# Kernel tuning notes

Hardware: AMD Instinct MI355X
Metric: run time of the kernel (lower is better)

The kernel has to match this reference:

```python
import jax, jax.numpy as jnp
import numpy as np
from jax import lax

B, CIN, H, W = 8, 256, 128, 128
CC, COUT = 16, 64
KH, KW = 5, 5
PT, PB = KH // 2, (KH + 1) // 2 - 1  # top/bottom pad (SAME-style)
PL, PR = KW // 2, (KW + 1) // 2 - 1


def setup_inputs() -> dict:
    key = jax.random.key(0)
    k1, k2, k3, k4 = jax.random.split(key, 4)
    x = jax.random.normal(k1, (B, CIN, H, W), dtype=jnp.float32)
    W_ext = jax.random.normal(k2, (CC, CIN, 3, 3), dtype=jnp.float32) * 0.05
    b_ext = jax.random.normal(k3, (CC,), dtype=jnp.float32) * 0.05
    W_reg = jax.random.normal(k4, (COUT, CC, KH, KW), dtype=jnp.float32) * 0.05
    return {"x": x, "W_ext": W_ext, "b_ext": b_ext, "W_reg": W_reg}


def reference(x, W_ext, b_ext, W_reg):
    # extract_input: Conv2d(in->corr_channels, 3x3, pad=1)
    f = lax.conv_general_dilated(
        x, W_ext, window_strides=(1, 1), padding=[(1, 1), (1, 1)],
        dimension_numbers=("NCHW", "OIHW", "NCHW"))
    f = f + b_ext[None, :, None, None]  # (B, CC, H, W)

    # Local autocorrelation: corr[b,c,h,w,di,dj] = f[b,c,h,w] * f_pad[b,c,h+di,w+dj]
    fp = jnp.pad(f, ((0, 0), (0, 0), (PT, PB), (PL, PR)))
    # stack shifted views over the fixed kh*kw offsets (small constant loop)
    patches = jnp.stack(
        [fp[:, :, i:i + H, j:j + W] for i in range(KH) for j in range(KW)],
        axis=-1)  # (B, CC, H, W, KH*KW)
    corr = f[..., None] * patches  # (B, CC, H, W, KH*KW) cost volume

    vec = jnp.einsum("bchwk,ock->bohw", corr, W_reg.reshape(COUT, CC, KH * KW))
    return vec  # (B, COUT, H, W)
```

## Files before the change

kernel.cpp:

```cpp
#include <hip/hip_runtime.h>

#define B_    8
#define CIN_  256
#define H_    128
#define W_    128
#define CC_   16
#define COUT_ 64
#define HFP_  132
#define HW_   (H_ * W_)

#define XS_STRIDE 1634
#define XS_BUF    (4 * XS_STRIDE)

typedef _Float16 half8 __attribute__((ext_vector_type(8)));
typedef float float4v __attribute__((ext_vector_type(4)));

__global__ void repack_w1(const float* __restrict__ Wext, _Float16* __restrict__ Wa1) {
    int i = blockIdx.x * 256 + threadIdx.x;
    if (i >= 9 * 8 * 64 * 8) return;
    int j    = i & 7;
    int lane = (i >> 3) & 63;
    int blk  = (i >> 9) & 7;
    int tap  = i >> 12;
    int cc   = lane & 15;
    int cin  = blk * 32 + (lane >> 4) * 8 + j;
    Wa1[i] = (_Float16)Wext[cc * (CIN_ * 9) + cin * 9 + tap];
}

__global__ void repack_w2(const float* __restrict__ Wreg, _Float16* __restrict__ Wa2) {
    int u = blockIdx.x * 256 + threadIdx.x;
    if (u >= 4 * 13 * 64 * 8) return;
    int j    = u & 7;
    int lane = (u >> 3) & 63;
    int su   = u >> 9;
    int s    = su % 13;
    int g    = su / 13;
    int q    = lane >> 4;
    int kk   = 2 * s + (q >> 1);
    int c    = (q & 1) * 8 + j;
    int o    = g * 16 + (lane & 15);
    float v  = (kk < 25) ? Wreg[o * (CC_ * 25) + c * 25 + kk] : 0.0f;
    Wa2[u] = (_Float16)v;
}

__global__ __launch_bounds__(256, 4) void conv_fused(
    const float* __restrict__ x, const _Float16* __restrict__ Wa1,
    const float* __restrict__ bext, _Float16* __restrict__ fpad)
{
    __shared__ _Float16 xs[2 * XS_BUF];
    __shared__ _Float16 lt[4][32][16];

    const int lane = threadIdx.x;
    const int wv   = threadIdx.y;
    const int tid  = wv * 64 + lane;
    const int n    = lane & 15;
    const int q    = lane >> 4;

    const int f  = blockIdx.x + 4 * blockIdx.y + 128 * blockIdx.z;
    const int b  = f & 7;
    const int wt = (f >> 3) & 3;
    const int ht = f >> 5;
    const int h0 = ht * 4;
    const int w0 = wt * 32;

    int  goff[4];
    int  loff[4];
    bool vld[4];
    bool act[4];
#pragma unroll
    for (int p = 0; p < 4; ++p) {
        int u = p * 256 + tid;
        act[p] = (u < 816);
        if (!act[p]) u = 0;
        const int col  = u % 34;
        const int pair = u / 34;
        const int row  = pair % 6;
        const int c8   = pair / 6;
        const int hh = h0 - 1 + row;
        const int ww = w0 - 1 + col;
        vld[p] = (hh >= 0) && (hh < H_) && (ww >= 0) && (ww < W_);
        const int hc = hh < 0 ? 0 : (hh > H_ - 1 ? H_ - 1 : hh);
        const int wc = ww < 0 ? 0 : (ww > W_ - 1 ? W_ - 1 : ww);
        goff[p] = (c8 * 8) * HW_ + hc * W_ + wc;
        loff[p] = c8 * XS_STRIDE + (row * 34 + col) * 8;
    }

    const float* xb = x + (size_t)b * (CIN_ * HW_);
    float4v acc[2] = {};

#pragma unroll
    for (int p = 0; p < 4; ++p) {
        if (act[p]) {
            half8 hv;
#pragma unroll
            for (int j = 0; j < 8; ++j) {
                const float v = xb[goff[p] + j * HW_];
                hv[j] = (_Float16)(vld[p] ? v : 0.0f);
            }
            *(half8*)(xs + loff[p]) = hv;
        }
    }

    float pf[4][8];
    for (int chunk = 0; chunk < 8; ++chunk) {
        __syncthreads();
        const int cur = chunk & 1;

        if (chunk < 7) {
            const float* xc = xb + (size_t)(chunk + 1) * (32 * HW_);
#pragma unroll
            for (int p = 0; p < 4; ++p) {
                if (act[p]) {
#pragma unroll
                    for (int j = 0; j < 8; ++j)
                        pf[p][j] = xc[goff[p] + j * HW_];
                }
            }
            __builtin_amdgcn_sched_barrier(0);
        }

        const _Float16* wchunk = Wa1 + (size_t)chunk * 512 + lane * 8;
        const _Float16* xsb    = xs + cur * XS_BUF + q * XS_STRIDE + (wv * 34 + n) * 8;
#pragma unroll
        for (int r = 0; r < 3; ++r) {
#pragma unroll
            for (int s = 0; s < 3; ++s) {
                const half8 af = *(const half8*)(wchunk + (r * 3 + s) * 4096);
#pragma unroll
                for (int st = 0; st < 2; ++st) {
                    const half8 bf = *(const half8*)(xsb + (r * 34 + s + st * 16) * 8);
                    acc[st] = __builtin_amdgcn_mfma_f32_16x16x32_f16(af, bf, acc[st], 0, 0, 0);
                }
            }
        }

        if (chunk < 7) {
            _Float16* xd = xs + (cur ^ 1) * XS_BUF;
#pragma unroll
            for (int p = 0; p < 4; ++p) {
                if (act[p]) {
                    half8 hv;
#pragma unroll
                    for (int j = 0; j < 8; ++j)
                        hv[j] = (_Float16)(vld[p] ? pf[p][j] : 0.0f);
                    *(half8*)(xd + loff[p]) = hv;
                }
            }
        }
    }

    float bias[4];
#pragma unroll
    for (int rr = 0; rr < 4; ++rr) bias[rr] = bext[q * 4 + rr];

#pragma unroll
    for (int st = 0; st < 2; ++st) {
#pragma unroll
        for (int rr = 0; rr < 4; ++rr) {
            lt[wv][st * 16 + n][q * 4 + rr] = (_Float16)(acc[st][rr] + bias[rr]);
        }
    }
    __syncthreads();

    const half8 o = *(const half8*)&lt[wv][lane >> 1][(lane & 1) * 8];
    _Float16* dst = fpad + (((size_t)b * HFP_ + (h0 + wv + 2)) * HFP_ + (w0 + (lane >> 1) + 2)) * 16
                    + (lane & 1) * 8;
    *(half8*)dst = o;
}

__global__ __launch_bounds__(256, 4) void corr_mfma(
    const _Float16* __restrict__ fpad, const _Float16* __restrict__ Wa2,
    float* __restrict__ out)
{
    const int lane = threadIdx.x;
    const int wv   = threadIdx.y;
    const int n    = lane & 15;
    const int q    = lane >> 4;

    const int f  = blockIdx.x + 2 * blockIdx.y + 256 * blockIdx.z;
    const int b  = f & 7;
    const int xt = (f >> 3) & 1;
    const int h  = f >> 4;
    const int w0 = xt * 64 + wv * 16;

    const _Float16* fb = fpad + ((size_t)b * HFP_ + h) * (HFP_ * 16);
    const int coff = (q & 1) * 8;

    const half8 ctr = *(const half8*)(fb + (size_t)(2 * HFP_ + (w0 + n + 2)) * 16 + coff);
    half8 sh[13];
#pragma unroll
    for (int s = 0; s < 13; ++s) {
        int kk = 2 * s + (q >> 1);
        if (kk > 24) kk = 24;
        const int ki = kk / 5, kj = kk % 5;
        sh[s] = *(const half8*)(fb + (size_t)(ki * HFP_ + (w0 + n + kj)) * 16 + coff);
    }
    __builtin_amdgcn_sched_barrier(0);

    half8 corr[13];
#pragma unroll
    for (int s = 0; s < 13; ++s) corr[s] = ctr * sh[s];

    float4v acc[4] = {};
    const _Float16* wp = Wa2 + (size_t)lane * 8;
#pragma unroll
    for (int s = 0; s < 13; ++s) {
#pragma unroll
        for (int g = 0; g < 4; ++g) {
            const half8 wf = *(const half8*)(wp + (size_t)(g * 13 + s) * 512);
            acc[g] = __builtin_amdgcn_mfma_f32_16x16x32_f16(wf, corr[s], acc[g], 0, 0, 0);
        }
    }

#pragma unroll
    for (int g = 0; g < 4; ++g) {
#pragma unroll
        for (int rr = 0; rr < 4; ++rr) {
            const int o = g * 16 + q * 4 + rr;
            out[((size_t)(b * COUT_ + o) * H_ + h) * W_ + (w0 + n)] = acc[g][rr];
        }
    }
}

extern "C" void kernel_launch(void* const* d_in, const int* in_sizes, int n_in,
                              void* d_out, int out_size, void* d_ws, size_t ws_size,
                              hipStream_t stream) {
    const float* x    = (const float*)d_in[0];
    const float* Wext = (const float*)d_in[1];
    const float* bext = (const float*)d_in[2];
    const float* Wreg = (const float*)d_in[3];
    float* out = (float*)d_out;

    char* ws = (char*)d_ws;
    _Float16* fpad = (_Float16*)ws;
    _Float16* Wa1  = (_Float16*)(ws + 4460544);
    _Float16* Wa2  = (_Float16*)(ws + 4460544 + 73728);

    repack_w1<<<dim3(144), dim3(256), 0, stream>>>(Wext, Wa1);
    repack_w2<<<dim3(104), dim3(256), 0, stream>>>(Wreg, Wa2);
    hipMemsetAsync(fpad, 0, (size_t)B_ * CC_ * HFP_ * HFP_ * sizeof(_Float16), stream);

    conv_fused<<<dim3(4, 32, 8), dim3(64, 4), 0, stream>>>(x, Wa1, bext, fpad);
    corr_mfma<<<dim3(2, 128, 8), dim3(64, 4), 0, stream>>>(fpad, Wa2, out);
}
```

Measured before the change: 272.2 us.

## Pre-convert input to padded fp16 channel-interleaved layout and stream via global_load_lds

```diff
diff --git a/kernel.cpp b/kernel.cpp
--- a/kernel.cpp
+++ b/kernel.cpp
@@ -8,12 +8,175 @@
 #define COUT_ 64
 #define HFP_  132
 #define HW_   (H_ * W_)
+#define XHP_  130
+#define XH_IMG   ((size_t)32 * XHP_ * XHP_ * 8)
+#define XH_CHUNK (4 * XHP_ * XHP_ * 8)
 
 #define XS_STRIDE 1634
 #define XS_BUF    (4 * XS_STRIDE)
 
 typedef _Float16 half8 __attribute__((ext_vector_type(8)));
 typedef float float4v __attribute__((ext_vector_type(4)));
+
+__device__ __forceinline__ void gload16(const _Float16* g, _Float16* l) {
+    __builtin_amdgcn_global_load_lds(
+        (const __attribute__((address_space(1))) void*)g,
+        (__attribute__((address_space(3))) void*)l, 16, 0, 0);
+}
+
+__global__ __launch_bounds__(256) void prep(
+    const float* __restrict__ x, const float* __restrict__ Wext,
+    const float* __restrict__ Wreg, _Float16* __restrict__ xh,
+    _Float16* __restrict__ Wa1, _Float16* __restrict__ Wa2,
+    _Float16* __restrict__ fpad)
+{
+    const int bid = blockIdx.x;
+    const int t   = threadIdx.x;
+    if (bid < 16384) {
+        const int task = bid * 2 + (t >> 7);
+        const int img  = task >> 12;
+        const int rem  = task & 4095;
+        const int c8   = rem >> 7;
+        const int h    = rem & 127;
+        const int w    = t & 127;
+        const float* xp = x + ((size_t)(img * 256 + c8 * 8)) * HW_ + h * W_ + w;
+        half8 hv;
+#pragma unroll
+        for (int j = 0; j < 8; ++j) hv[j] = (_Float16)xp[j * HW_];
+        *(half8*)(xh + ((((size_t)img * 32 + c8) * XHP_ + (h + 1)) * XHP_ + (w + 1)) * 8) = hv;
+    } else if (bid < 16900) {
+        const int e  = (bid - 16384) * 256 + t;
+        const int ic = e / 516;
+        const int pe = e % 516;
+        const int img = ic >> 5, c8 = ic & 31;
+        int hp, wp;
+        if (pe < 130)      { hp = 0;              wp = pe; }
+        else if (pe < 260) { hp = 129;            wp = pe - 130; }
+        else if (pe < 388) { hp = 1 + (pe - 260); wp = 0; }
+        else               { hp = 1 + (pe - 388); wp = 129; }
+        half8 z = {};
+        *(half8*)(xh + ((((size_t)img * 32 + c8) * XHP_ + hp) * XHP_ + wp) * 8) = z;
+    } else if (bid < 16965) {
+        const int e = (bid - 16900) * 256 + t;
+        if (e < 16640) {
+            const int img = e / 2080;
+            const int r   = e % 2080;
+            const int pxi = r >> 1, hf = r & 1;
+            int hp, wp;
+            if (pxi < 264)      { hp = pxi / 132;                wp = pxi % 132; }
+            else if (pxi < 528) { int pz = pxi - 264; hp = 130 + pz / 132; wp = pz % 132; }
+            else { int q2 = pxi - 528; hp = 2 + (q2 >> 2); int s2 = q2 & 3;
+                   wp = (s2 < 2) ? s2 : 128 + (s2 - 2); }
+            half8 z = {};
+            *(half8*)(fpad + (((size_t)img * HFP_ + hp) * HFP_ + wp) * 16 + hf * 8) = z;
+        }
+    } else if (bid < 17109) {
+        const int i = (bid - 16965) * 256 + t;
+        const int j = i & 7, lane = (i >> 3) & 63, blk = (i >> 9) & 7, tap = i >> 12;
+        const int cc  = lane & 15;
+        const int cin = blk * 32 + (lane >> 4) * 8 + j;
+        Wa1[i] = (_Float16)Wext[cc * (CIN_ * 9) + cin * 9 + tap];
+    } else {
+        const int u = (bid - 17109) * 256 + t;
+        const int j = u & 7, lane = (u >> 3) & 63;
+        const int su = u >> 9, s = su % 13, g = su / 13;
+        const int q = lane >> 4;
+        int kk = 2 * s + (q >> 1);
+        const int c = (q & 1) * 8 + j;
+        const int o = g * 16 + (lane & 15);
+        float v = (kk < 25) ? Wreg[o * (CC_ * 25) + c * 25 + kk] : 0.0f;
+        Wa2[u] = (_Float16)v;
+    }
+}
+
+__global__ __launch_bounds__(256, 4) void conv_fused2(
+    const _Float16* __restrict__ xh, const _Float16* __restrict__ Wa1,
+    const float* __restrict__ bext, _Float16* __restrict__ fpad)
+{
+    __shared__ _Float16 xs[2 * 6528];
+    __shared__ _Float16 lt[4][32][16];
+
+    const int lane = threadIdx.x;
+    const int wv   = threadIdx.y;
+    const int n    = lane & 15;
+    const int q    = lane >> 4;
+
+    const int f  = blockIdx.x + 4 * blockIdx.y + 128 * blockIdx.z;
+    const int b  = f & 7;
+    const int wt = (f >> 3) & 3;
+    const int ht = f >> 5;
+    const int h0 = ht * 4;
+    const int w0 = wt * 32;
+
+    const _Float16* xhb = xh + (size_t)b * XH_IMG;
+    const _Float16* g[4];
+#pragma unroll
+    for (int k = 0; k < 4; ++k) {
+        int u = wv * 204 + k * 64 + lane;
+        if (k == 3 && lane >= 12) u = wv * 204;
+        const int c8  = u / 204;
+        const int rem = u % 204;
+        const int row = rem / 34;
+        const int col = rem % 34;
+        g[k] = xhb + (((size_t)c8 * XHP_ + (h0 + row)) * XHP_ + (w0 + col)) * 8;
+    }
+
+#pragma unroll
+    for (int k = 0; k < 4; ++k) {
+        if (k < 3 || lane < 12) gload16(g[k], xs + (wv * 204 + k * 64) * 8);
+        g[k] += XH_CHUNK;
+    }
+    asm volatile("s_waitcnt vmcnt(0)" ::: "memory");
+
+    float4v acc[2] = {};
+    for (int chunk = 0; chunk < 8; ++chunk) {
+        __syncthreads();
+        const int cur = chunk & 1;
+
+        if (chunk < 7) {
+            _Float16* xd = xs + (cur ^ 1) * 6528;
+#pragma unroll
+            for (int k = 0; k < 4; ++k) {
+                if (k < 3 || lane < 12) gload16(g[k], xd + (wv * 204 + k * 64) * 8);
+                g[k] += XH_CHUNK;
+            }
+        }
+
+        const _Float16* wchunk = Wa1 + (size_t)chunk * 512 + lane * 8;
+        const _Float16* xsb    = xs + cur * 6528 + ((q * 6 + wv) * 34 + n) * 8;
+#pragma unroll
+        for (int r = 0; r < 3; ++r) {
+#pragma unroll
+            for (int s = 0; s < 3; ++s) {
+                const half8 af = *(const half8*)(wchunk + (r * 3 + s) * 4096);
+#pragma unroll
+                for (int st = 0; st < 2; ++st) {
+                    const half8 bf = *(const half8*)(xsb + (r * 34 + s + st * 16) * 8);
+                    acc[st] = __builtin_amdgcn_mfma_f32_16x16x32_f16(af, bf, acc[st], 0, 0, 0);
+                }
+            }
+        }
+        asm volatile("s_waitcnt vmcnt(0)" ::: "memory");
+    }
+
+    float bias[4];
+#pragma unroll
+    for (int rr = 0; rr < 4; ++rr) bias[rr] = bext[q * 4 + rr];
+
+#pragma unroll
+    for (int st = 0; st < 2; ++st) {
+#pragma unroll
+        for (int rr = 0; rr < 4; ++rr) {
+            lt[wv][st * 16 + n][q * 4 + rr] = (_Float16)(acc[st][rr] + bias[rr]);
+        }
+    }
+    __syncthreads();
+
+    const half8 o = *(const half8*)&lt[wv][lane >> 1][(lane & 1) * 8];
+    _Float16* dst = fpad + (((size_t)b * HFP_ + (h0 + wv + 2)) * HFP_ + (w0 + (lane >> 1) + 2)) * 16
+                    + (lane & 1) * 8;
+    *(half8*)dst = o;
+}
 
 __global__ void repack_w1(const float* __restrict__ Wext, _Float16* __restrict__ Wa1) {
     int i = blockIdx.x * 256 + threadIdx.x;
@@ -116,7 +279,6 @@
                         pf[p][j] = xc[goff[p] + j * HW_];
                 }
             }
-            __builtin_amdgcn_sched_barrier(0);
         }
 
         const _Float16* wchunk = Wa1 + (size_t)chunk * 512 + lane * 8;
@@ -235,11 +397,19 @@
     _Float16* fpad = (_Float16*)ws;
     _Float16* Wa1  = (_Float16*)(ws + 4460544);
     _Float16* Wa2  = (_Float16*)(ws + 4460544 + 73728);
-
-    repack_w1<<<dim3(144), dim3(256), 0, stream>>>(Wext, Wa1);
-    repack_w2<<<dim3(104), dim3(256), 0, stream>>>(Wreg, Wa2);
-    hipMemsetAsync(fpad, 0, (size_t)B_ * CC_ * HFP_ * HFP_ * sizeof(_Float16), stream);
-
-    conv_fused<<<dim3(4, 32, 8), dim3(64, 4), 0, stream>>>(x, Wa1, bext, fpad);
-    corr_mfma<<<dim3(2, 128, 8), dim3(64, 4), 0, stream>>>(fpad, Wa2, out);
-}
+    const size_t XH_OFF = 4460544 + 73728 + 53248;
+    const size_t XH_B   = (size_t)8 * 32 * XHP_ * XHP_ * 8 * 2;
+
+    if (ws_size >= XH_OFF + XH_B) {
+        _Float16* xh = (_Float16*)(ws + XH_OFF);
+        prep<<<dim3(17213), dim3(256), 0, stream>>>(x, Wext, Wreg, xh, Wa1, Wa2, fpad);
+        conv_fused2<<<dim3(4, 32, 8), dim3(64, 4), 0, stream>>>(xh, Wa1, bext, fpad);
+        corr_mfma<<<dim3(2, 128, 8), dim3(64, 4), 0, stream>>>(fpad, Wa2, out);
+    } else {
+        repack_w1<<<dim3(144), dim3(256), 0, stream>>>(Wext, Wa1);
+        repack_w2<<<dim3(104), dim3(256), 0, stream>>>(Wreg, Wa2);
+        hipMemsetAsync(fpad, 0, (size_t)B_ * CC_ * HFP_ * HFP_ * sizeof(_Float16), stream);
+        conv_fused<<<dim3(4, 32, 8), dim3(64, 4), 0, stream>>>(x, Wa1, bext, fpad);
+        corr_mfma<<<dim3(2, 128, 8), dim3(64, 4), 0, stream>>>(fpad, Wa2, out);
+    }
+}
```

After: 246.4 us. 9.5% less time.
